# Kernel optimization log

Measured on AMD Instinct MI355X. Metric: run time of the kernel, lower is better.

The kernel has to match this reference:

```python
import jax, jax.numpy as jnp
import numpy as np

BS, NQ, NK = 2, 2048, 2048
D_OUT, H, D_K, D_V = 1024, 16, 64, 64


def _xavier(key, shape):
    fan_in, fan_out = shape[1], shape[0]
    lim = float(np.sqrt(6.0 / (fan_in + fan_out)))
    return jax.random.uniform(key, shape, jnp.float32, -lim, lim)


def setup_inputs() -> dict:
    key = jax.random.key(0)
    ks = jax.random.split(key, 9)
    return {
        "queries": jax.random.normal(ks[0], (BS, NQ, D_OUT), jnp.float32),
        "keys": jax.random.normal(ks[1], (BS, NK, D_OUT), jnp.float32),
        "values": jax.random.normal(ks[2], (BS, NK, D_OUT), jnp.float32),
        "mask": jax.random.randint(ks[3], (BS, H, NQ, NK), 0, 2).astype(bool),
        "weights": jax.random.uniform(ks[4], (BS, H, NQ, NK), jnp.float32),
        "Wq": _xavier(ks[5], (H * D_K, D_OUT)),
        "bq": jnp.zeros((H * D_K,), jnp.float32),
        "Wk": _xavier(ks[6], (H * D_K, D_OUT)),
        "bk": jnp.zeros((H * D_K,), jnp.float32),
        "Wv": _xavier(ks[7], (H * D_V, D_OUT)),
        "bv": jnp.zeros((H * D_V,), jnp.float32),
        "Wo": _xavier(ks[8], (D_OUT, H * D_V)),
        "bo": jnp.zeros((D_OUT,), jnp.float32),
    }


def reference(queries, keys, values, mask, weights, Wq, bq, Wk, bk, Wv, bv, Wo, bo):
    bs, nq, _ = queries.shape
    nk = keys.shape[1]
    # projections: (bs, n, h*d) -> (bs, h, n, d)
    q = (queries @ Wq.T + bq).reshape(bs, nq, H, D_K).transpose(0, 2, 1, 3)
    k = (keys @ Wk.T + bk).reshape(bs, nk, H, D_K).transpose(0, 2, 1, 3)
    v = (values @ Wv.T + bv).reshape(bs, nk, H, D_V).transpose(0, 2, 1, 3)
    # scaled dot-product scores: (bs, h, nq, nk)
    att = jnp.einsum("bhqd,bhkd->bhqk", q, k) / jnp.sqrt(jnp.float32(D_K))
    att = att * weights                      # elementwise weight bias
    att = jnp.where(mask, -jnp.inf, att)     # masked_fill(mask, -inf)
    att = jax.nn.softmax(att, axis=-1)
    # dropout is identity at p=0 / eval
    out = jnp.einsum("bhqk,bhkd->bhqd", att, v)  # (bs, h, nq, d_v)
    out = out.transpose(0, 2, 1, 3).reshape(bs, nq, H * D_V)
    return out @ Wo.T + bo
```

## Files before the change

kernel.cpp:

```cpp
#include <hip/hip_runtime.h>
#include <stdint.h>

#define DEV __device__ __forceinline__

typedef __attribute__((__ext_vector_type__(8))) short short8;
typedef __attribute__((__ext_vector_type__(4))) float f32x4;
typedef __attribute__((__ext_vector_type__(4))) unsigned short ushort4_t;

DEV unsigned short f2bf(float f) {
  union { float f; unsigned u; } x; x.f = f;
  unsigned u = x.u;
  unsigned r = (u + 0x7FFFu + ((u >> 16) & 1u)) >> 16;
  return (unsigned short)r;
}

DEV void gload_lds16(const void* g, void* l) {
  __builtin_amdgcn_global_load_lds(
      (const __attribute__((address_space(1))) unsigned int*)g,
      (__attribute__((address_space(3))) unsigned int*)l,
      16, 0, 0);
}

DEV short8 ld_g8(const unsigned short* p) { return *(const short8*)p; }
DEV short8 ld_s8(const unsigned short* p) { return *(const short8*)p; }

__global__ void detect_mask_fmt(const unsigned int* __restrict__ mask, int* __restrict__ flag) {
  if (threadIdx.x == 0 && blockIdx.x == 0) {
    int fmt = 1;
    for (int i = 0; i < 256; ++i) {
      unsigned u = mask[i];
      if (u == 0x3F800000u) { fmt = 2; break; }
      if ((u & 0xFFFFFF00u) != 0u) { fmt = 0; break; }
    }
    *flag = fmt;
  }
}

__global__ void cvt_all(const float* __restrict__ q, const float* __restrict__ k,
                        const float* __restrict__ v,
                        const float* __restrict__ wq, const float* __restrict__ wk,
                        const float* __restrict__ wv, const float* __restrict__ wo,
                        unsigned short* __restrict__ Xq, unsigned short* __restrict__ Xk,
                        unsigned short* __restrict__ Xv, unsigned short* __restrict__ Wqb,
                        unsigned short* __restrict__ Wkb, unsigned short* __restrict__ Wvb,
                        unsigned short* __restrict__ Wob) {
  int i = blockIdx.x * 256 + threadIdx.x;
  const float* src; unsigned short* dst; int off;
  if (i < 1048576)      { src = q;  dst = Xq;  off = i; }
  else if (i < 2097152) { src = k;  dst = Xk;  off = i - 1048576; }
  else if (i < 3145728) { src = v;  dst = Xv;  off = i - 2097152; }
  else if (i < 3407872) { src = wq; dst = Wqb; off = i - 3145728; }
  else if (i < 3670016) { src = wk; dst = Wkb; off = i - 3407872; }
  else if (i < 3932160) { src = wv; dst = Wvb; off = i - 3670016; }
  else                  { src = wo; dst = Wob; off = i - 3932160; }
  float4 vv = ((const float4*)src)[off];
  ushort4_t r;
  r.x = f2bf(vv.x); r.y = f2bf(vv.y); r.z = f2bf(vv.z); r.w = f2bf(vv.w);
  ((ushort4_t*)dst)[off] = r;
}

__global__ __launch_bounds__(256, 2) void proj_gemm(
    const unsigned short* __restrict__ Xq, const unsigned short* __restrict__ Xk,
    const unsigned short* __restrict__ Xv,
    const unsigned short* __restrict__ Wqb, const unsigned short* __restrict__ Wkb,
    const unsigned short* __restrict__ Wvb,
    const float* __restrict__ bq, const float* __restrict__ bk, const float* __restrict__ bv,
    unsigned short* __restrict__ QP, unsigned short* __restrict__ KP,
    unsigned short* __restrict__ VT) {
  const int tid = threadIdx.x;
  const int wid = tid >> 6, lane = tid & 63;
  const int l16 = lane & 15, hi = lane >> 4;
  const int m0 = blockIdx.x * 128;
  const int sel = blockIdx.y >> 3;
  const int n0 = (blockIdx.y & 7) * 128;

  const unsigned short* X; const unsigned short* W; const float* bias; unsigned short* out;
  if (sel == 0)      { X = Xq; W = Wqb; bias = bq; out = QP; }
  else if (sel == 1) { X = Xk; W = Wkb; bias = bk; out = KP; }
  else               { X = Xv; W = Wvb; bias = bv; out = VT; }

  __shared__ unsigned short stage[2 * 128 * 32];

  f32x4 acc[4][4] = {};
  const int wm = (wid >> 1) * 64, wn = (wid & 1) * 64;
  const int aoff = (sel == 2) ? 4096 : 0;
  const int boff = 4096 - aoff;

  for (int kt = 0; kt < 1024; kt += 32) {
#pragma unroll
    for (int t = 0; t < 4; ++t) {
      int g = wid * 4 + t;
      int c = g & 7;
      int row = c * 16 + (lane >> 2);
      int ko = (lane & 3) * 8;
      const unsigned short* src = (g < 8)
          ? (X + (size_t)(m0 + row) * 1024 + kt + ko)
          : (W + (size_t)(n0 + row) * 1024 + kt + ko);
      gload_lds16(src, (unsigned short*)((char*)stage + g * 1024));
    }
    __syncthreads();

    short8 af[4], bfr[4];
#pragma unroll
    for (int i = 0; i < 4; ++i)
      af[i] = ld_s8(&stage[aoff + (wm + i * 16 + l16) * 32 + hi * 8]);
#pragma unroll
    for (int j = 0; j < 4; ++j)
      bfr[j] = ld_s8(&stage[boff + (wn + j * 16 + l16) * 32 + hi * 8]);
#pragma unroll
    for (int i = 0; i < 4; ++i)
#pragma unroll
      for (int j = 0; j < 4; ++j)
        acc[i][j] = __builtin_amdgcn_mfma_f32_16x16x32_bf16(af[i], bfr[j], acc[i][j], 0, 0, 0);
    __syncthreads();
  }

  if (sel != 2) {
#pragma unroll
    for (int j = 0; j < 4; ++j) {
      int feat = n0 + wn + j * 16 + l16;
      float bi = bias[feat];
      int h = feat >> 6, d = feat & 63;
#pragma unroll
      for (int i = 0; i < 4; ++i) {
#pragma unroll
        for (int r = 0; r < 4; ++r) {
          int m = m0 + wm + i * 16 + hi * 4 + r;
          int b = m >> 11, n = m & 2047;
          float v = acc[i][j][r] + bi;
          out[(((size_t)(b * 16 + h)) * 2048 + n) * 64 + d] = f2bf(v);
        }
      }
    }
  } else {
#pragma unroll
    for (int j = 0; j < 4; ++j) {
      int tc0 = m0 + wn + j * 16;
      int b = tc0 >> 11, n = tc0 & 2047;
#pragma unroll
      for (int i = 0; i < 4; ++i) {
#pragma unroll
        for (int r = 0; r < 4; ++r) {
          int feat = n0 + wm + i * 16 + hi * 4 + r;
          int h = feat >> 6, d = feat & 63;
          float v = acc[i][j][r] + bias[feat];
          out[((size_t)(b * 16 + h) * 64 + d) * 2048 + n + l16] = f2bf(v);
        }
      }
    }
  }
}

__global__ __launch_bounds__(256, 3) void attn_kernel(
    const unsigned short* __restrict__ Q, const unsigned short* __restrict__ K,
    const unsigned short* __restrict__ VT,
    const float* __restrict__ weights,
    const unsigned char* __restrict__ mask8, const unsigned int* __restrict__ mask32,
    const int* __restrict__ mfmt,
    unsigned short* __restrict__ O) {
  const int bid = blockIdx.x;
  const int r8 = bid & 7, g = bid >> 3;
  const int qt = g & 31, bh = r8 + 8 * (g >> 5);
  const int b = bh >> 4, h = bh & 15;
  const int tid = threadIdx.x, wid = tid >> 6, lane = tid & 63;
  const int l16 = lane & 15, hi = lane >> 4;
  const size_t bh_nd = (size_t)bh * 2048 * 64;
  const size_t bh_nn = (size_t)bh * 2048 * 2048;
  const int q0 = qt * 64;
  const int qrow_frag = q0 + wid * 16 + l16;
  const int qrow_d = q0 + wid * 16 + hi * 4;
  const int fmt = *mfmt;
  const bool m4 = (fmt != 0);

  short8 qf[2];
  qf[0] = ld_g8(Q + bh_nd + (size_t)qrow_frag * 64 + hi * 8);
  qf[1] = ld_g8(Q + bh_nd + (size_t)qrow_frag * 64 + 32 + hi * 8);

  __shared__ unsigned short vTd[2][64 * 32];
  __shared__ unsigned short plds[4][16 * 40];

  const int vd = wid * 16 + (lane >> 2);
  const int vko = (lane & 3) * 8;
  const unsigned short* vsrc = VT + bh_nd + (size_t)vd * 2048 + vko;

  const size_t wm_base = bh_nn + (size_t)qrow_d * 2048 + l16;

  f32x4 o[4] = {};
  float mrow[4], lrow[4];
#pragma unroll
  for (int r = 0; r < 4; ++r) { mrow[r] = -1e30f; lrow[r] = 0.f; }

  float wA[8], wB[8];
  unsigned mbA = 0, mbB = 0;

#define LOADWM(WW, MB, T)                                                  \
  {                                                                        \
    unsigned _mb = 0;                                                      \
    if (m4) {                                                              \
      _Pragma("unroll") for (int c0 = 0; c0 < 2; ++c0)                     \
      _Pragma("unroll") for (int r = 0; r < 4; ++r) {                      \
        size_t idx = wm_base + (size_t)r * 2048 + (T) * 32 + c0 * 16;      \
        WW[c0 * 4 + r] = 0.125f * weights[idx];                            \
        _mb |= (mask32[idx] ? 1u : 0u) << (c0 * 4 + r);                    \
      }                                                                    \
    } else {                                                               \
      _Pragma("unroll") for (int c0 = 0; c0 < 2; ++c0)                     \
      _Pragma("unroll") for (int r = 0; r < 4; ++r) {                      \
        size_t idx = wm_base + (size_t)r * 2048 + (T) * 32 + c0 * 16;      \
        WW[c0 * 4 + r] = 0.125f * weights[idx];                            \
        _mb |= (mask8[idx] ? 1u : 0u) << (c0 * 4 + r);                     \
      }                                                                    \
    }                                                                      \
    MB = _mb;                                                              \
  }

#define STEP(T, CUR, NXT, WC, MBC, WN, MBN)                                \
  {                                                                        \
    const int kt0 = (T) * 32;                                              \
    if ((T) + 1 < 64)                                                      \
      gload_lds16(vsrc + (size_t)(kt0 + 32),                               \
                  (unsigned short*)((char*)vTd[NXT] + wid * 1024));        \
                                                   \
    f32x4 s[2];                                                            \
    _Pragma("unroll") for (int c0 = 0; c0 < 2; ++c0) {                     \
      f32x4 z = {};                                                        \
      short8 k0 = ld_g8(K + bh_nd + (size_t)(kt0 + c0 * 16 + l16) * 64 + hi * 8); \
      short8 k1 = ld_g8(K + bh_nd + (size_t)(kt0 + c0 * 16 + l16) * 64 + 32 + hi * 8); \
      z = __builtin_amdgcn_mfma_f32_16x16x32_bf16(qf[0], k0, z, 0, 0, 0);  \
      z = __builtin_amdgcn_mfma_f32_16x16x32_bf16(qf[1], k1, z, 0, 0, 0);  \
      s[c0] = z;                                                           \
    }                                                                      \
    if ((T) + 1 < 64) LOADWM(WN, MBN, (T) + 1)                             \
                                                 \
    _Pragma("unroll") for (int c0 = 0; c0 < 2; ++c0)                       \
    _Pragma("unroll") for (int r = 0; r < 4; ++r)                          \
      s[c0][r] = ((MBC >> (c0 * 4 + r)) & 1) ? -INFINITY                   \
                                             : s[c0][r] * WC[c0 * 4 + r];  \
                                                       \
    float tmax[4];                                                         \
    _Pragma("unroll") for (int r = 0; r < 4; ++r)                          \
      tmax[r] = fmaxf(s[0][r], s[1][r]);                                   \
    _Pragma("unroll") for (int msk = 1; msk < 16; msk <<= 1)               \
    _Pragma("unroll") for (int r = 0; r < 4; ++r)                          \
      tmax[r] = fmaxf(tmax[r], __shfl_xor(tmax[r], msk));                  \
    _Pragma("unroll") for (int r = 0; r < 4; ++r) {                        \
      float mnew = fmaxf(mrow[r], tmax[r]);                                \
      float sc = __expf(mrow[r] - mnew);                                   \
      mrow[r] = mnew; lrow[r] *= sc;                                       \
      _Pragma("unroll") for (int d0 = 0; d0 < 4; ++d0) o[d0][r] *= sc;     \
    }                                                                      \
    float psum[4];                                                         \
    _Pragma("unroll") for (int r = 0; r < 4; ++r) {                        \
      s[0][r] = __expf(s[0][r] - mrow[r]);                                 \
      s[1][r] = __expf(s[1][r] - mrow[r]);                                 \
      psum[r] = s[0][r] + s[1][r];                                         \
    }                                                                      \
    _Pragma("unroll") for (int msk = 1; msk < 16; msk <<= 1)               \
    _Pragma("unroll") for (int r = 0; r < 4; ++r)                          \
      psum[r] += __shfl_xor(psum[r], msk);                                 \
    _Pragma("unroll") for (int r = 0; r < 4; ++r) lrow[r] += psum[r];      \
                                          \
    _Pragma("unroll") for (int c0 = 0; c0 < 2; ++c0)                       \
    _Pragma("unroll") for (int r = 0; r < 4; ++r)                          \
      plds[wid][(hi * 4 + r) * 40 + c0 * 16 + l16] = f2bf(s[c0][r]);       \
    short8 pa = ld_s8(&plds[wid][l16 * 40 + hi * 8]);                      \
    _Pragma("unroll") for (int d0 = 0; d0 < 4; ++d0) {                     \
      short8 vb = ld_s8(&vTd[CUR][(d0 * 16 + l16) * 32 + hi * 8]);         \
      o[d0] = __builtin_amdgcn_mfma_f32_16x16x32_bf16(pa, vb, o[d0], 0, 0, 0); \
    }                                                                      \
    __syncthreads();                                                       \
  }

  LOADWM(wA, mbA, 0)
  gload_lds16(vsrc, (unsigned short*)((char*)vTd[0] + wid * 1024));
  __syncthreads();

  for (int t = 0; t < 64; t += 2) {
    STEP(t,     0, 1, wA, mbA, wB, mbB)
    STEP(t + 1, 1, 0, wB, mbB, wA, mbA)
  }

#pragma unroll
  for (int r = 0; r < 4; ++r) {
    float inv = 1.0f / lrow[r];
    int row = qrow_d + r;
#pragma unroll
    for (int d0 = 0; d0 < 4; ++d0)
      O[((size_t)(b * 2048 + row)) * 1024 + h * 64 + d0 * 16 + l16] = f2bf(o[d0][r] * inv);
  }
#undef STEP
#undef LOADWM
}

__global__ __launch_bounds__(256, 2) void out_gemm(
    const unsigned short* __restrict__ A, const unsigned short* __restrict__ W,
    const float* __restrict__ bias, float* __restrict__ Cout) {
  const int tid = threadIdx.x;
  const int wid = tid >> 6, lane = tid & 63;
  const int l16 = lane & 15, hi = lane >> 4;
  const int m0 = blockIdx.x * 128;
  const int n0 = blockIdx.y * 128;

  __shared__ unsigned short stage[2 * 128 * 32];
  f32x4 acc[4][4] = {};
  const int wm = (wid >> 1) * 64, wn = (wid & 1) * 64;

  for (int kt = 0; kt < 1024; kt += 32) {
#pragma unroll
    for (int t = 0; t < 4; ++t) {
      int g = wid * 4 + t;
      int c = g & 7;
      int row = c * 16 + (lane >> 2);
      int ko = (lane & 3) * 8;
      const unsigned short* src = (g < 8)
          ? (A + (size_t)(m0 + row) * 1024 + kt + ko)
          : (W + (size_t)(n0 + row) * 1024 + kt + ko);
      gload_lds16(src, (unsigned short*)((char*)stage + g * 1024));
    }
    __syncthreads();

    short8 af[4], bfr[4];
#pragma unroll
    for (int i = 0; i < 4; ++i)
      af[i] = ld_s8(&stage[(wm + i * 16 + l16) * 32 + hi * 8]);
#pragma unroll
    for (int j = 0; j < 4; ++j)
      bfr[j] = ld_s8(&stage[4096 + (wn + j * 16 + l16) * 32 + hi * 8]);
#pragma unroll
    for (int i = 0; i < 4; ++i)
#pragma unroll
      for (int j = 0; j < 4; ++j)
        acc[i][j] = __builtin_amdgcn_mfma_f32_16x16x32_bf16(af[i], bfr[j], acc[i][j], 0, 0, 0);
    __syncthreads();
  }

#pragma unroll
  for (int j = 0; j < 4; ++j) {
    int feat = n0 + wn + j * 16 + l16;
    float bi = bias[feat];
#pragma unroll
    for (int i = 0; i < 4; ++i) {
#pragma unroll
      for (int r = 0; r < 4; ++r) {
        int m = m0 + wm + i * 16 + hi * 4 + r;
        Cout[(size_t)m * 1024 + feat] = acc[i][j][r] + bi;
      }
    }
  }
}

extern "C" void kernel_launch(void* const* d_in, const int* in_sizes, int n_in,
                              void* d_out, int out_size, void* d_ws, size_t ws_size,
                              hipStream_t stream) {
  const float* queries = (const float*)d_in[0];
  const float* keys    = (const float*)d_in[1];
  const float* values  = (const float*)d_in[2];
  const void*  maskp   = d_in[3];
  const float* weights = (const float*)d_in[4];
  const float* Wq = (const float*)d_in[5];
  const float* bq = (const float*)d_in[6];
  const float* Wk = (const float*)d_in[7];
  const float* bk = (const float*)d_in[8];
  const float* Wv = (const float*)d_in[9];
  const float* bv = (const float*)d_in[10];
  const float* Wo = (const float*)d_in[11];
  const float* bo = (const float*)d_in[12];

  unsigned short* ws = (unsigned short*)d_ws;
  unsigned short* Xq  = ws;
  unsigned short* Xk  = ws + 4194304;
  unsigned short* Xv  = ws + 8388608;
  unsigned short* Wqb = ws + 12582912;
  unsigned short* Wkb = ws + 13631488;
  unsigned short* Wvb = ws + 14680064;
  unsigned short* Wob = ws + 15728640;
  unsigned short* QP  = ws + 16777216;
  unsigned short* KP  = ws + 20971520;
  unsigned short* VPT = ws + 25165824;
  unsigned short* OB  = Xq;
  int* mflag = (int*)(ws + 29360128);

  detect_mask_fmt<<<1, 64, 0, stream>>>((const unsigned int*)maskp, mflag);

  cvt_all<<<16384, 256, 0, stream>>>(queries, keys, values, Wq, Wk, Wv, Wo,
                                     Xq, Xk, Xv, Wqb, Wkb, Wvb, Wob);

  proj_gemm<<<dim3(32, 24), 256, 0, stream>>>(Xq, Xk, Xv, Wqb, Wkb, Wvb,
                                              bq, bk, bv, QP, KP, VPT);
  attn_kernel<<<1024, 256, 0, stream>>>(
      QP, KP, VPT, weights,
      (const unsigned char*)maskp, (const unsigned int*)maskp, mflag, OB);
  out_gemm<<<dim3(32, 8), 256, 0, stream>>>(OB, Wob, bo, (float*)d_out);
}
```

Measured before the change: 377.1 us.

## Stage weights/mask/V tiles into swizzled LDS and transpose score MFMA layout

Rewrites the attention inner loop to compute S transposed (K as the A operand), so each lane owns one query row and the row max and sum need only two cross-lane shuffles. The weights, the byte mask and V tiles are now double-buffered into XOR-swizzled LDS through direct global-to-LDS loads, replacing per-lane scattered global loads. P·V now uses fp16 16x16x16 MFMA with P kept in registers, which removes the P round trip through LDS, and the V projection output is switched to fp16. Occupancy is raised to 4 blocks per SM. In exchange the kernel uses more LDS and takes on fp16 range and precision risk for V.

```diff
diff --git a/kernel.cpp b/kernel.cpp
--- a/kernel.cpp
+++ b/kernel.cpp
@@ -4,14 +4,25 @@
 #define DEV __device__ __forceinline__
 
 typedef __attribute__((__ext_vector_type__(8))) short short8;
+typedef __attribute__((__ext_vector_type__(4))) short short4_t;
 typedef __attribute__((__ext_vector_type__(4))) float f32x4;
 typedef __attribute__((__ext_vector_type__(4))) unsigned short ushort4_t;
+typedef __attribute__((__ext_vector_type__(4))) _Float16 half4;
+
+#define MFMA16F16(a, b, c) __builtin_amdgcn_mfma_f32_16x16x16f16((a), (b), (c), 0, 0, 0)
 
 DEV unsigned short f2bf(float f) {
   union { float f; unsigned u; } x; x.f = f;
   unsigned u = x.u;
   unsigned r = (u + 0x7FFFu + ((u >> 16) & 1u)) >> 16;
   return (unsigned short)r;
+}
+
+DEV unsigned short f2h(float f) {
+  _Float16 h = (_Float16)f;
+  unsigned short u;
+  __builtin_memcpy(&u, &h, 2);
+  return u;
 }
 
 DEV void gload_lds16(const void* g, void* l) {
@@ -144,14 +155,14 @@
           int feat = n0 + wm + i * 16 + hi * 4 + r;
           int h = feat >> 6, d = feat & 63;
           float v = acc[i][j][r] + bias[feat];
-          out[((size_t)(b * 16 + h) * 64 + d) * 2048 + n + l16] = f2bf(v);
+          out[((size_t)(b * 16 + h) * 64 + d) * 2048 + n + l16] = f2h(v);
         }
       }
     }
   }
 }
 
-__global__ __launch_bounds__(256, 3) void attn_kernel(
+__global__ __launch_bounds__(256, 4) void attn_kernel(
     const unsigned short* __restrict__ Q, const unsigned short* __restrict__ K,
     const unsigned short* __restrict__ VT,
     const float* __restrict__ weights,
@@ -167,129 +178,137 @@
   const size_t bh_nd = (size_t)bh * 2048 * 64;
   const size_t bh_nn = (size_t)bh * 2048 * 2048;
   const int q0 = qt * 64;
-  const int qrow_frag = q0 + wid * 16 + l16;
-  const int qrow_d = q0 + wid * 16 + hi * 4;
+  const int qloc = wid * 16 + l16;
   const int fmt = *mfmt;
-  const bool m4 = (fmt != 0);
+  const bool staged_mask = (fmt == 0);
 
   short8 qf[2];
-  qf[0] = ld_g8(Q + bh_nd + (size_t)qrow_frag * 64 + hi * 8);
-  qf[1] = ld_g8(Q + bh_nd + (size_t)qrow_frag * 64 + 32 + hi * 8);
-
-  __shared__ unsigned short vTd[2][64 * 32];
-  __shared__ unsigned short plds[4][16 * 40];
-
-  const int vd = wid * 16 + (lane >> 2);
-  const int vko = (lane & 3) * 8;
-  const unsigned short* vsrc = VT + bh_nd + (size_t)vd * 2048 + vko;
-
-  const size_t wm_base = bh_nn + (size_t)qrow_d * 2048 + l16;
+  qf[0] = ld_g8(Q + bh_nd + (size_t)(q0 + qloc) * 64 + hi * 8);
+  qf[1] = ld_g8(Q + bh_nd + (size_t)(q0 + qloc) * 64 + 32 + hi * 8);
+
+  __shared__ float wlds[2][64 * 32];
+  __shared__ unsigned short vlds[2][64 * 32];
+  __shared__ unsigned char mlds[2][64 * 32];
+
+  const int wr8 = lane >> 3;
+  const int wcu = (lane & 7) ^ wr8;
+  const size_t woff0 = (size_t)(q0 + wid * 16 + wr8) * 2048 + 4 * wcu;
+  const int vr = (lane >> 2) & 15;
+  const int vcu = (lane & 3) ^ (vr & 3);
+  const size_t voff = (size_t)(wid * 16 + vr) * 2048 + 8 * vcu;
+  const int mr = lane >> 1;
+  const int mcu = (lane & 1) ^ (mr & 1);
+  const size_t moff = (size_t)(q0 + wid * 32 + mr) * 2048 + 16 * mcu;
+
+  const float* wsrc = weights + bh_nn;
+  const unsigned short* vsrc = VT + bh_nd;
+  const unsigned char* msrc = mask8 + bh_nn;
+
+#define STAGE(NXT, KT)                                                         \
+  {                                                                            \
+    gload_lds16(wsrc + woff0 + (KT), &wlds[NXT][wid * 512]);                   \
+    gload_lds16(wsrc + woff0 + 8 * 2048 + (KT), &wlds[NXT][wid * 512 + 256]);  \
+    gload_lds16(vsrc + voff + (KT), &vlds[NXT][wid * 512]);                    \
+    if (staged_mask && wid < 2)                                                \
+      gload_lds16(msrc + moff + (KT), &mlds[NXT][wid * 1024]);                 \
+  }
 
   f32x4 o[4] = {};
-  float mrow[4], lrow[4];
-#pragma unroll
-  for (int r = 0; r < 4; ++r) { mrow[r] = -1e30f; lrow[r] = 0.f; }
-
-  float wA[8], wB[8];
-  unsigned mbA = 0, mbB = 0;
-
-#define LOADWM(WW, MB, T)                                                  \
-  {                                                                        \
-    unsigned _mb = 0;                                                      \
-    if (m4) {                                                              \
-      _Pragma("unroll") for (int c0 = 0; c0 < 2; ++c0)                     \
-      _Pragma("unroll") for (int r = 0; r < 4; ++r) {                      \
-        size_t idx = wm_base + (size_t)r * 2048 + (T) * 32 + c0 * 16;      \
-        WW[c0 * 4 + r] = 0.125f * weights[idx];                            \
-        _mb |= (mask32[idx] ? 1u : 0u) << (c0 * 4 + r);                    \
-      }                                                                    \
-    } else {                                                               \
-      _Pragma("unroll") for (int c0 = 0; c0 < 2; ++c0)                     \
-      _Pragma("unroll") for (int r = 0; r < 4; ++r) {                      \
-        size_t idx = wm_base + (size_t)r * 2048 + (T) * 32 + c0 * 16;      \
-        WW[c0 * 4 + r] = 0.125f * weights[idx];                            \
-        _mb |= (mask8[idx] ? 1u : 0u) << (c0 * 4 + r);                     \
-      }                                                                    \
-    }                                                                      \
-    MB = _mb;                                                              \
-  }
-
-#define STEP(T, CUR, NXT, WC, MBC, WN, MBN)                                \
-  {                                                                        \
-    const int kt0 = (T) * 32;                                              \
-    if ((T) + 1 < 64)                                                      \
-      gload_lds16(vsrc + (size_t)(kt0 + 32),                               \
-                  (unsigned short*)((char*)vTd[NXT] + wid * 1024));        \
-                                                   \
-    f32x4 s[2];                                                            \
-    _Pragma("unroll") for (int c0 = 0; c0 < 2; ++c0) {                     \
-      f32x4 z = {};                                                        \
-      short8 k0 = ld_g8(K + bh_nd + (size_t)(kt0 + c0 * 16 + l16) * 64 + hi * 8); \
-      short8 k1 = ld_g8(K + bh_nd + (size_t)(kt0 + c0 * 16 + l16) * 64 + 32 + hi * 8); \
-      z = __builtin_amdgcn_mfma_f32_16x16x32_bf16(qf[0], k0, z, 0, 0, 0);  \
-      z = __builtin_amdgcn_mfma_f32_16x16x32_bf16(qf[1], k1, z, 0, 0, 0);  \
-      s[c0] = z;                                                           \
-    }                                                                      \
-    if ((T) + 1 < 64) LOADWM(WN, MBN, (T) + 1)                             \
-                                                 \
-    _Pragma("unroll") for (int c0 = 0; c0 < 2; ++c0)                       \
-    _Pragma("unroll") for (int r = 0; r < 4; ++r)                          \
-      s[c0][r] = ((MBC >> (c0 * 4 + r)) & 1) ? -INFINITY                   \
-                                             : s[c0][r] * WC[c0 * 4 + r];  \
-                                                       \
-    float tmax[4];                                                         \
-    _Pragma("unroll") for (int r = 0; r < 4; ++r)                          \
-      tmax[r] = fmaxf(s[0][r], s[1][r]);                                   \
-    _Pragma("unroll") for (int msk = 1; msk < 16; msk <<= 1)               \
-    _Pragma("unroll") for (int r = 0; r < 4; ++r)                          \
-      tmax[r] = fmaxf(tmax[r], __shfl_xor(tmax[r], msk));                  \
-    _Pragma("unroll") for (int r = 0; r < 4; ++r) {                        \
-      float mnew = fmaxf(mrow[r], tmax[r]);                                \
-      float sc = __expf(mrow[r] - mnew);                                   \
-      mrow[r] = mnew; lrow[r] *= sc;                                       \
-      _Pragma("unroll") for (int d0 = 0; d0 < 4; ++d0) o[d0][r] *= sc;     \
-    }                                                                      \
-    float psum[4];                                                         \
-    _Pragma("unroll") for (int r = 0; r < 4; ++r) {                        \
-      s[0][r] = __expf(s[0][r] - mrow[r]);                                 \
-      s[1][r] = __expf(s[1][r] - mrow[r]);                                 \
-      psum[r] = s[0][r] + s[1][r];                                         \
-    }                                                                      \
-    _Pragma("unroll") for (int msk = 1; msk < 16; msk <<= 1)               \
-    _Pragma("unroll") for (int r = 0; r < 4; ++r)                          \
-      psum[r] += __shfl_xor(psum[r], msk);                                 \
-    _Pragma("unroll") for (int r = 0; r < 4; ++r) lrow[r] += psum[r];      \
-                                          \
-    _Pragma("unroll") for (int c0 = 0; c0 < 2; ++c0)                       \
-    _Pragma("unroll") for (int r = 0; r < 4; ++r)                          \
-      plds[wid][(hi * 4 + r) * 40 + c0 * 16 + l16] = f2bf(s[c0][r]);       \
-    short8 pa = ld_s8(&plds[wid][l16 * 40 + hi * 8]);                      \
-    _Pragma("unroll") for (int d0 = 0; d0 < 4; ++d0) {                     \
-      short8 vb = ld_s8(&vTd[CUR][(d0 * 16 + l16) * 32 + hi * 8]);         \
-      o[d0] = __builtin_amdgcn_mfma_f32_16x16x32_bf16(pa, vb, o[d0], 0, 0, 0); \
-    }                                                                      \
-    __syncthreads();                                                       \
-  }
-
-  LOADWM(wA, mbA, 0)
-  gload_lds16(vsrc, (unsigned short*)((char*)vTd[0] + wid * 1024));
+  float mrow = -1e30f, lrow = 0.f;
+
+  STAGE(0, 0)
   __syncthreads();
 
-  for (int t = 0; t < 64; t += 2) {
-    STEP(t,     0, 1, wA, mbA, wB, mbB)
-    STEP(t + 1, 1, 0, wB, mbB, wA, mbA)
-  }
-
-#pragma unroll
-  for (int r = 0; r < 4; ++r) {
-    float inv = 1.0f / lrow[r];
-    int row = qrow_d + r;
-#pragma unroll
-    for (int d0 = 0; d0 < 4; ++d0)
-      O[((size_t)(b * 2048 + row)) * 1024 + h * 64 + d0 * 16 + l16] = f2bf(o[d0][r] * inv);
-  }
-#undef STEP
-#undef LOADWM
+  for (int t = 0; t < 64; ++t) {
+    const int cur = t & 1;
+    const int kt0 = t * 32;
+
+    short8 kf00 = ld_g8(K + bh_nd + (size_t)(kt0 + l16) * 64 + hi * 8);
+    short8 kf01 = ld_g8(K + bh_nd + (size_t)(kt0 + l16) * 64 + 32 + hi * 8);
+    short8 kf10 = ld_g8(K + bh_nd + (size_t)(kt0 + 16 + l16) * 64 + hi * 8);
+    short8 kf11 = ld_g8(K + bh_nd + (size_t)(kt0 + 16 + l16) * 64 + 32 + hi * 8);
+
+    if (t < 63) STAGE(cur ^ 1, kt0 + 32)
+
+    f32x4 s0 = {}, s1 = {};
+    s0 = __builtin_amdgcn_mfma_f32_16x16x32_bf16(kf00, qf[0], s0, 0, 0, 0);
+    s0 = __builtin_amdgcn_mfma_f32_16x16x32_bf16(kf01, qf[1], s0, 0, 0, 0);
+    s1 = __builtin_amdgcn_mfma_f32_16x16x32_bf16(kf10, qf[0], s1, 0, 0, 0);
+    s1 = __builtin_amdgcn_mfma_f32_16x16x32_bf16(kf11, qf[1], s1, 0, 0, 0);
+
+    f32x4 w0 = *(const f32x4*)&wlds[cur][qloc * 32 + 4 * ((hi + 0) ^ (l16 & 7))];
+    f32x4 w1 = *(const f32x4*)&wlds[cur][qloc * 32 + 4 * ((hi + 4) ^ (l16 & 7))];
+    unsigned mv0, mv1;
+    if (staged_mask) {
+      mv0 = *(const unsigned*)&mlds[cur][qloc * 32 + 16 * (0 ^ (l16 & 1)) + 4 * hi];
+      mv1 = *(const unsigned*)&mlds[cur][qloc * 32 + 16 * (1 ^ (l16 & 1)) + 4 * hi];
+    } else {
+      mv0 = mv1 = 0;
+      const size_t mb = bh_nn + (size_t)(q0 + qloc) * 2048 + kt0 + 4 * hi;
+#pragma unroll
+      for (int r = 0; r < 4; ++r) {
+        mv0 |= (mask32[mb + r] ? 0xFFu : 0u) << (8 * r);
+        mv1 |= (mask32[mb + 16 + r] ? 0xFFu : 0u) << (8 * r);
+      }
+    }
+#pragma unroll
+    for (int r = 0; r < 4; ++r) {
+      s0[r] = ((mv0 >> (8 * r)) & 0xFF) ? -INFINITY : s0[r] * 0.125f * w0[r];
+      s1[r] = ((mv1 >> (8 * r)) & 0xFF) ? -INFINITY : s1[r] * 0.125f * w1[r];
+    }
+
+    float tm = fmaxf(fmaxf(fmaxf(s0[0], s0[1]), fmaxf(s0[2], s0[3])),
+                     fmaxf(fmaxf(s1[0], s1[1]), fmaxf(s1[2], s1[3])));
+    tm = fmaxf(tm, __shfl_xor(tm, 16));
+    tm = fmaxf(tm, __shfl_xor(tm, 32));
+    float mnew = fmaxf(mrow, tm);
+    float sc = __expf(mrow - mnew);
+    mrow = mnew;
+    lrow *= sc;
+#pragma unroll
+    for (int d0 = 0; d0 < 4; ++d0) {
+      o[d0][0] *= sc; o[d0][1] *= sc; o[d0][2] *= sc; o[d0][3] *= sc;
+    }
+#pragma unroll
+    for (int r = 0; r < 4; ++r) {
+      s0[r] = __expf(s0[r] - mrow);
+      s1[r] = __expf(s1[r] - mrow);
+    }
+    float ps = s0[0] + s0[1] + s0[2] + s0[3] + s1[0] + s1[1] + s1[2] + s1[3];
+    ps += __shfl_xor(ps, 16);
+    ps += __shfl_xor(ps, 32);
+    lrow += ps;
+
+    half4 p0, p1;
+    p0[0] = (_Float16)s0[0]; p0[1] = (_Float16)s0[1];
+    p0[2] = (_Float16)s0[2]; p0[3] = (_Float16)s0[3];
+    p1[0] = (_Float16)s1[0]; p1[1] = (_Float16)s1[1];
+    p1[2] = (_Float16)s1[2]; p1[3] = (_Float16)s1[3];
+
+#pragma unroll
+    for (int d0 = 0; d0 < 4; ++d0) {
+      union { short4_t s; half4 h; } v0, v1;
+      v0.s = *(const short4_t*)&vlds[cur][(d0 * 16 + l16) * 32 +
+              8 * ((2 * 0 + (hi >> 1)) ^ (l16 & 3)) + 4 * (hi & 1)];
+      v1.s = *(const short4_t*)&vlds[cur][(d0 * 16 + l16) * 32 +
+              8 * ((2 * 1 + (hi >> 1)) ^ (l16 & 3)) + 4 * (hi & 1)];
+      o[d0] = MFMA16F16(v0.h, p0, o[d0]);
+      o[d0] = MFMA16F16(v1.h, p1, o[d0]);
+    }
+
+    __syncthreads();
+  }
+
+  float inv = 1.0f / lrow;
+  const size_t obase = (size_t)(b * 2048 + q0 + qloc) * 1024 + h * 64;
+#pragma unroll
+  for (int d0 = 0; d0 < 4; ++d0) {
+    ushort4_t pk;
+    pk.x = f2bf(o[d0][0] * inv); pk.y = f2bf(o[d0][1] * inv);
+    pk.z = f2bf(o[d0][2] * inv); pk.w = f2bf(o[d0][3] * inv);
+    *(ushort4_t*)&O[obase + d0 * 16 + 4 * hi] = pk;
+  }
+#undef STAGE
 }
 
 __global__ __launch_bounds__(256, 2) void out_gemm(
```

New measurement: 387.2 us. 1.03x slower.
